# Optimization experiments

Measured on AMD Instinct MI355X. Metric: run time of the kernel, lower is better.

The kernel has to match this reference:

```python
import jax, jax.numpy as jnp
import numpy as np

B, N, DIM, H, HD, MLP = 32, 257, 1024, 16, 64, 4096
SCALE = HD ** -0.5


def _ln(x, w, b, eps=1e-5):
    m = x.mean(-1, keepdims=True)
    v = ((x - m) ** 2).mean(-1, keepdims=True)
    return (x - m) * jax.lax.rsqrt(v + eps) * w + b


def _quick_gelu(x):
    return x * jax.nn.sigmoid(1.702 * x)


def setup_inputs() -> dict:
    key = jax.random.key(0)
    ks = jax.random.split(key, 8)
    p = lambda k, s: jax.random.normal(k, s, jnp.float32) * 0.02
    return {
        'hidden_states': jax.random.normal(ks[0], (B, N, DIM), jnp.float32),
        'ln1_w': jnp.ones((DIM,), jnp.float32), 'ln1_b': jnp.zeros((DIM,), jnp.float32),
        'Wq': p(ks[1], (DIM, DIM)), 'bq': jnp.zeros((DIM,), jnp.float32),
        'Wk': p(ks[2], (DIM, DIM)), 'bk': jnp.zeros((DIM,), jnp.float32),
        'Wv': p(ks[3], (DIM, DIM)), 'bv': jnp.zeros((DIM,), jnp.float32),
        'Wo': p(ks[4], (DIM, DIM)), 'bo': jnp.zeros((DIM,), jnp.float32),
        'ln2_w': jnp.ones((DIM,), jnp.float32), 'ln2_b': jnp.zeros((DIM,), jnp.float32),
        'fc1_w': p(ks[5], (MLP, DIM)), 'fc1_b': jnp.zeros((MLP,), jnp.float32),
        'fc2_w': p(ks[6], (DIM, MLP)), 'fc2_b': jnp.zeros((DIM,), jnp.float32),
    }


def reference(hidden_states, ln1_w, ln1_b, Wq, bq, Wk, bk, Wv, bv, Wo, bo,
              ln2_w, ln2_b, fc1_w, fc1_b, fc2_w, fc2_b):
    x = _ln(hidden_states, ln1_w, ln1_b)            # [B,N,DIM]
    def heads(y):                                    # [B,N,DIM] -> [B,H,N,HD]
        return y.reshape(B, N, H, HD).transpose(0, 2, 1, 3)
    q = heads((x @ Wq.T + bq) * SCALE)
    k = heads(x @ Wk.T + bk)
    v = heads(x @ Wv.T + bv)
    attn_weights = jax.nn.softmax(jnp.einsum('bhnd,bhmd->bhnm', q, k), axis=-1)  # [B,H,N,N]
    ctx = jnp.einsum('bhnm,bhmd->bhnd', attn_weights, v)
    pre_proj = ctx.transpose(0, 2, 1, 3).reshape(B, N, DIM)
    attn_output = pre_proj @ Wo.T + bo
    h = hidden_states + attn_output
    residual = h
    h = _ln(h, ln2_w, ln2_b)
    h = _quick_gelu(h @ fc1_w.T + fc1_b) @ fc2_w.T + fc2_b
    hidden_out = residual + h
    # reuse_start='before_mlp': returns (pre_proj, cache_states=None, hidden, attn_weights, qkvs=None, reuse_map=None)
    return pre_proj, hidden_out, attn_weights
```

## Files before the change

kernel.cpp:

```cpp
#include <hip/hip_runtime.h>

typedef unsigned short u16;
typedef __bf16 bf16x8 __attribute__((ext_vector_type(8)));
typedef float f32x4 __attribute__((ext_vector_type(4)));
typedef unsigned short u16x8 __attribute__((ext_vector_type(8)));
typedef unsigned short u16x4 __attribute__((ext_vector_type(4)));

#define NBATCH 32
#define NTOK   257
#define DMODEL 1024
#define NHEAD  16
#define HDIM   64
#define DMLP   4096
#define MTOK   (NBATCH*NTOK)
#define MPAD   8320

__device__ __forceinline__ u16 f2bf(float f){
    unsigned int u = __float_as_uint(f);
    u = u + 0x7fffu + ((u >> 16) & 1u);
    return (u16)(u >> 16);
}

__device__ __forceinline__ f32x4 mfma16(bf16x8 a, bf16x8 b, f32x4 c){
    return __builtin_amdgcn_mfma_f32_16x16x32_bf16(a, b, c, 0, 0, 0);
}

__device__ __forceinline__ void gload16(const void* g, void* l){
    __builtin_amdgcn_global_load_lds(
        (const __attribute__((address_space(1))) unsigned int*)g,
        (__attribute__((address_space(3))) unsigned int*)l, 16, 0, 0);
}

__device__ __forceinline__ float waveSum64(float v){
    #pragma unroll
    for (int d = 1; d < 64; d <<= 1) v += __shfl_xor(v, d);
    return v;
}

__device__ __forceinline__ void xcd_swz(int &bx, int &by){
    int gx = gridDim.x;
    int nwg = gx * gridDim.y;
    int bid = blockIdx.y * gx + blockIdx.x;
    int wg = (bid & 7) * (nwg >> 3) + (bid >> 3);
    bx = wg % gx; by = wg / gx;
}

__global__ __launch_bounds__(256) void cvt_all(
        const float* __restrict__ wq, const float* __restrict__ wk,
        const float* __restrict__ wv, const float* __restrict__ wo,
        const float* __restrict__ f1, const float* __restrict__ f2,
        u16* __restrict__ dst){
    int b = blockIdx.x;
    const float* s; int rb; float sc = 1.0f;
    if (b < 1024)      { s = wq; rb = 0;    sc = 0.125f; }
    else if (b < 2048) { s = wk; rb = 1024; }
    else if (b < 3072) { s = wv; rb = 2048; }
    else if (b < 4096) { s = wo; rb = 3072; }
    else if (b < 8192) { s = f1; rb = 4096; }
    else               { s = f2; rb = 8192; }
    size_t li = ((size_t)(b - rb)*256 + threadIdx.x)*4;
    float4 v = *(const float4*)(s + li);
    u16x4 o = { f2bf(v.x*sc), f2bf(v.y*sc), f2bf(v.z*sc), f2bf(v.w*sc) };
    *(u16x4*)(dst + (size_t)b*1024 + threadIdx.x*4) = o;
}

__global__ __launch_bounds__(256) void build_bqkv(
        const float* __restrict__ bq, const float* __restrict__ bk,
        const float* __restrict__ bv, float* __restrict__ o){
    int i = blockIdx.x*256 + threadIdx.x;
    float v = (i < 1024) ? bq[i]*0.125f : ((i < 2048) ? bk[i-1024] : bv[i-2048]);
    o[i] = v;
}

__global__ __launch_bounds__(256) void ln_kernel(const float* __restrict__ x,
                                                 const float* __restrict__ w,
                                                 const float* __restrict__ b,
                                                 u16* __restrict__ y){
    int row = blockIdx.x, tid = threadIdx.x;
    float4 v = ((const float4*)(x + (size_t)row*DMODEL))[tid];
    float s = v.x + v.y + v.z + v.w;
    s = waveSum64(s);
    __shared__ float red[8];
    int wv = tid >> 6;
    if ((tid & 63) == 0) red[wv] = s;
    __syncthreads();
    float mean = (red[0]+red[1]+red[2]+red[3]) * (1.0f/1024.0f);
    float dx = v.x-mean, dy = v.y-mean, dz = v.z-mean, dw = v.w-mean;
    float s2 = dx*dx + dy*dy + dz*dz + dw*dw;
    s2 = waveSum64(s2);
    if ((tid & 63) == 0) red[4+wv] = s2;
    __syncthreads();
    float var = (red[4]+red[5]+red[6]+red[7]) * (1.0f/1024.0f);
    float rs = rsqrtf(var + 1e-5f);
    float4 wl = ((const float4*)w)[tid];
    float4 bl = ((const float4*)b)[tid];
    u16x4 o = { f2bf(dx*rs*wl.x + bl.x), f2bf(dy*rs*wl.y + bl.y),
                f2bf(dz*rs*wl.z + bl.z), f2bf(dw*rs*wl.w + bl.w) };
    ((u16x4*)(y + (size_t)row*DMODEL))[tid] = o;
}

template<int EPI>
__global__ __launch_bounds__(256) void gemm_bt(
        const u16* __restrict__ A, const u16* __restrict__ Wt,
        const float* __restrict__ bias, u16* __restrict__ outb,
        int K, int Nn, int Mvalid){
    __shared__ __align__(16) u16 As[128*64];
    __shared__ __align__(16) u16 Bs[128*64];
    int tid = threadIdx.x, lane = tid & 63, w = tid >> 6;
    int wr = w >> 1, wc = w & 1;
    int bx, by; xcd_swz(bx, by);
    int m0 = by*128, n0 = bx*128;
    int lrow = lane & 15, lk = lane >> 4;
    const f32x4 fz = {0.f,0.f,0.f,0.f};
    f32x4 acc[4][4];
    #pragma unroll
    for (int i = 0; i < 4; i++)
        #pragma unroll
        for (int j = 0; j < 4; j++) acc[i][j] = fz;

    const size_t Ks = (size_t)K;
    int so = w*1024 + lane*16;
    for (int kt = 0; kt < K; kt += 64){
        #pragma unroll
        for (int i = 0; i < 4; i++){
            int o = i*4096 + so;
            int row = o >> 7;
            int gsl = ((o >> 4) & 7) ^ (row & 7);
            gload16(A  + (size_t)(m0+row)*Ks + kt + gsl*8, &As[i*2048 + w*512]);
            gload16(Wt + (size_t)(n0+row)*Ks + kt + gsl*8, &Bs[i*2048 + w*512]);
        }
        __syncthreads();
        #pragma unroll
        for (int kk = 0; kk < 2; kk++){
            bf16x8 af[4], bfr[4];
            #pragma unroll
            for (int mi = 0; mi < 4; mi++){
                int row = wr*64 + mi*16 + lrow;
                int sl = (kk*4 + lk) ^ (row & 7);
                af[mi] = *(const bf16x8*)&As[row*64 + sl*8];
            }
            #pragma unroll
            for (int ni = 0; ni < 4; ni++){
                int row = wc*64 + ni*16 + lrow;
                int sl = (kk*4 + lk) ^ (row & 7);
                bfr[ni] = *(const bf16x8*)&Bs[row*64 + sl*8];
            }
            #pragma unroll
            for (int mi = 0; mi < 4; mi++)
                #pragma unroll
                for (int ni = 0; ni < 4; ni++)
                    acc[mi][ni] = mfma16(af[mi], bfr[ni], acc[mi][ni]);
        }
        __syncthreads();
    }
    #pragma unroll
    for (int mi = 0; mi < 4; mi++){
        #pragma unroll
        for (int ni = 0; ni < 4; ni++){
            int col = n0 + wc*64 + ni*16 + lrow;
            float bi = bias[col];
            #pragma unroll
            for (int r = 0; r < 4; r++){
                int row = m0 + wr*64 + mi*16 + lk*4 + r;
                if (row < Mvalid){
                    float v = acc[mi][ni][r] + bi;
                    size_t idx = (size_t)row*Nn + col;
                    if (EPI == 0){
                        outb[idx] = f2bf(v);
                    } else {
                        float g = v / (1.f + __expf(-1.702f*v));
                        outb[idx] = f2bf(g);
                    }
                }
            }
        }
    }
}

__global__ __launch_bounds__(256) void gemm_n64(
        const u16* __restrict__ A, const u16* __restrict__ Wt,
        const float* __restrict__ bias, const float* __restrict__ addsrc,
        float* __restrict__ outf,
        int K, int Nn, int Mvalid){
    __shared__ __align__(16) u16 As[128*64];
    __shared__ __align__(16) u16 Bs[64*64];
    int tid = threadIdx.x, lane = tid & 63, w = tid >> 6;
    int wr = w >> 1, wc = w & 1;
    int bx, by; xcd_swz(bx, by);
    int m0 = by*128, n0 = bx*64;
    int lrow = lane & 15, lk = lane >> 4;
    const f32x4 fz = {0.f,0.f,0.f,0.f};
    f32x4 acc[4][2];
    #pragma unroll
    for (int i = 0; i < 4; i++){ acc[i][0] = fz; acc[i][1] = fz; }

    const size_t Ks = (size_t)K;
    int so = w*1024 + lane*16;
    for (int kt = 0; kt < K; kt += 64){
        #pragma unroll
        for (int i = 0; i < 4; i++){
            int o = i*4096 + so;
            int row = o >> 7;
            int gsl = ((o >> 4) & 7) ^ (row & 7);
            gload16(A + (size_t)(m0+row)*Ks + kt + gsl*8, &As[i*2048 + w*512]);
        }
        #pragma unroll
        for (int i = 0; i < 2; i++){
            int o = i*4096 + so;
            int row = o >> 7;
            int gsl = ((o >> 4) & 7) ^ (row & 7);
            gload16(Wt + (size_t)(n0+row)*Ks + kt + gsl*8, &Bs[i*2048 + w*512]);
        }
        __syncthreads();
        #pragma unroll
        for (int kk = 0; kk < 2; kk++){
            bf16x8 af[4], bfr[2];
            #pragma unroll
            for (int mi = 0; mi < 4; mi++){
                int row = wr*64 + mi*16 + lrow;
                int sl = (kk*4 + lk) ^ (row & 7);
                af[mi] = *(const bf16x8*)&As[row*64 + sl*8];
            }
            #pragma unroll
            for (int ni = 0; ni < 2; ni++){
                int row = wc*32 + ni*16 + lrow;
                int sl = (kk*4 + lk) ^ (row & 7);
                bfr[ni] = *(const bf16x8*)&Bs[row*64 + sl*8];
            }
            #pragma unroll
            for (int mi = 0; mi < 4; mi++)
                #pragma unroll
                for (int ni = 0; ni < 2; ni++)
                    acc[mi][ni] = mfma16(af[mi], bfr[ni], acc[mi][ni]);
        }
        __syncthreads();
    }
    #pragma unroll
    for (int mi = 0; mi < 4; mi++){
        #pragma unroll
        for (int ni = 0; ni < 2; ni++){
            int col = n0 + wc*32 + ni*16 + lrow;
            float bi = bias[col];
            #pragma unroll
            for (int r = 0; r < 4; r++){
                int row = m0 + wr*64 + mi*16 + lk*4 + r;
                if (row < Mvalid){
                    float v = acc[mi][ni][r] + bi;
                    size_t idx = (size_t)row*Nn + col;
                    outf[idx] = addsrc[idx] + v;
                }
            }
        }
    }
}

__global__ __launch_bounds__(256) void attn_kernel(
        const u16* __restrict__ qkv, float* __restrict__ preproj,
        u16* __restrict__ ctxb, float* __restrict__ attnw){
    __shared__ __align__(16) u16 Klds[272*64];
    __shared__ __align__(16) u16 Vt[64*296];
    __shared__ __align__(16) u16 Plds[9*64*32];
    int tid = threadIdx.x, lane = tid & 63, w = tid >> 6;
    int bh = blockIdx.x, bq = bh >> 4, hh = bh & 15;
    int q0 = blockIdx.y*64;
    int lrow = lane & 15, lk = lane >> 4;

    size_t base3 = ((size_t)bq*NTOK)*3072 + hh*HDIM;
    for (int c = tid; c < 2176; c += 256){
        int row = c >> 3, slot = c & 7;
        u16x8 kv = {0,0,0,0,0,0,0,0}, vv = {0,0,0,0,0,0,0,0};
        if (row < NTOK){
            kv = *(const u16x8*)(qkv + base3 + 1024 + (size_t)row*3072 + slot*8);
            vv = *(const u16x8*)(qkv + base3 + 2048 + (size_t)row*3072 + slot*8);
        }
        *(u16x8*)&Klds[row*64 + (slot ^ (row & 7))*8] = kv;
        #pragma unroll
        for (int j = 0; j < 8; j++) Vt[(slot*8 + j)*296 + row] = vv[j];
    }
    for (int i = tid; i < 1024; i += 256) ((unsigned int*)Plds)[8*1024 + i] = 0u;
    for (int i = tid; i < 1536; i += 256){
        int d = i/24, c2 = 272 + (i - d*24);
        Vt[d*296 + c2] = 0;
    }
    int tok = bq*NTOK + q0 + w*16 + lrow;
    const u16* qp = qkv + (size_t)tok*3072 + hh*HDIM;
    bf16x8 qf0 = *(const bf16x8*)(qp + lk*8);
    bf16x8 qf1 = *(const bf16x8*)(qp + 32 + lk*8);
    __syncthreads();

    f32x4 S[17];
    #pragma unroll
    for (int j = 0; j < 17; j++){
        int kcol = j*16 + lrow;
        f32x4 a = {0.f,0.f,0.f,0.f};
        bf16x8 b0 = *(const bf16x8*)&Klds[kcol*64 + ((0 + lk) ^ (kcol & 7))*8];
        a = mfma16(qf0, b0, a);
        bf16x8 b1 = *(const bf16x8*)&Klds[kcol*64 + ((4 + lk) ^ (kcol & 7))*8];
        S[j] = mfma16(qf1, b1, a);
    }
    #pragma unroll
    for (int r = 0; r < 4; r++){
        float mx = -1e30f;
        #pragma unroll
        for (int j = 0; j < 17; j++){
            bool valid = (j < 16) || (lrow == 0);
            mx = fmaxf(mx, valid ? S[j][r] : -1e30f);
        }
        #pragma unroll
        for (int d = 1; d < 16; d <<= 1) mx = fmaxf(mx, __shfl_xor(mx, d));
        float sum = 0.f;
        #pragma unroll
        for (int j = 0; j < 17; j++){
            bool valid = (j < 16) || (lrow == 0);
            float p = valid ? __expf(S[j][r] - mx) : 0.f;
            S[j][r] = p; sum += p;
        }
        #pragma unroll
        for (int d = 1; d < 16; d <<= 1) sum += __shfl_xor(sum, d);
        float inv = 1.f / sum;
        #pragma unroll
        for (int j = 0; j < 17; j++) S[j][r] *= inv;
    }
    #pragma unroll
    for (int r = 0; r < 4; r++){
        int rw = lk*4 + r;
        int qrow = q0 + w*16 + rw;
        bool rowok = qrow < NTOK;
        size_t obase = ((size_t)bh*NTOK + qrow)*NTOK;
        int prow = w*16 + rw;
        #pragma unroll
        for (int j = 0; j < 17; j++){
            int col = j*16 + lrow;
            float p = S[j][r];
            if (rowok && col < NTOK) attnw[obase + col] = p;
            int kstep = col >> 5, koff = col & 31;
            int slot = (koff >> 3) ^ (prow & 3);
            Plds[kstep*2048 + prow*32 + slot*8 + (koff & 7)] = f2bf(p);
        }
    }
    __syncthreads();

    f32x4 C4[4];
    #pragma unroll
    for (int n = 0; n < 4; n++) C4[n] = (f32x4){0.f,0.f,0.f,0.f};
    #pragma unroll
    for (int ks = 0; ks < 9; ks++){
        int prow = w*16 + lrow;
        int slotp = lk ^ (prow & 3);
        bf16x8 pf = *(const bf16x8*)&Plds[ks*2048 + prow*32 + slotp*8];
        #pragma unroll
        for (int n = 0; n < 4; n++){
            int d = n*16 + lrow;
            bf16x8 vf = *(const bf16x8*)&Vt[d*296 + ks*32 + lk*8];
            C4[n] = mfma16(pf, vf, C4[n]);
        }
    }
    #pragma unroll
    for (int n = 0; n < 4; n++){
        #pragma unroll
        for (int r = 0; r < 4; r++){
            int qrow = q0 + w*16 + lk*4 + r;
            if (qrow < NTOK){
                int tok2 = bq*NTOK + qrow;
                int d = hh*HDIM + n*16 + lrow;
                float v = C4[n][r];
                preproj[(size_t)tok2*DMODEL + d] = v;
                ctxb[(size_t)tok2*DMODEL + d] = f2bf(v);
            }
        }
    }
}

extern "C" void kernel_launch(void* const* d_in, const int* in_sizes, int n_in,
                              void* d_out, int out_size, void* d_ws, size_t ws_size,
                              hipStream_t stream){
    const float* hidden = (const float*)d_in[0];
    const float* ln1w = (const float*)d_in[1];
    const float* ln1b = (const float*)d_in[2];
    const float* Wq   = (const float*)d_in[3];
    const float* bq   = (const float*)d_in[4];
    const float* Wk   = (const float*)d_in[5];
    const float* bk   = (const float*)d_in[6];
    const float* Wv   = (const float*)d_in[7];
    const float* bv   = (const float*)d_in[8];
    const float* Wo   = (const float*)d_in[9];
    const float* bo   = (const float*)d_in[10];
    const float* ln2w = (const float*)d_in[11];
    const float* ln2b = (const float*)d_in[12];
    const float* fc1w = (const float*)d_in[13];
    const float* fc1b = (const float*)d_in[14];
    const float* fc2w = (const float*)d_in[15];
    const float* fc2b = (const float*)d_in[16];

    float* out0 = (float*)d_out;
    float* out1 = out0 + (size_t)MTOK*DMODEL;
    float* out2 = out1 + (size_t)MTOK*DMODEL;

    char* ws = (char*)d_ws;
    u16* qkvb = (u16*)ws;
    u16* fc1o = (u16*)ws;
    size_t off = (size_t)MPAD*DMLP*2;
    u16* xln  = (u16*)(ws + off);
    u16* ctxb = xln;
    off += (size_t)MPAD*DMODEL*2;
    u16* wbase = (u16*)(ws + off);
    u16* wqkv = wbase;
    u16* wob  = wbase + 3*1048576;
    u16* wf1  = wbase + 4*1048576;
    u16* wf2  = wbase + 8*1048576;
    off += (size_t)12*1048576*2;
    float* bqkv = (float*)(ws + off);

    cvt_all<<<12288, 256, 0, stream>>>(Wq, Wk, Wv, Wo, fc1w, fc2w, wbase);
    build_bqkv<<<12, 256, 0, stream>>>(bq, bk, bv, bqkv);

    ln_kernel<<<MTOK, 256, 0, stream>>>(hidden, ln1w, ln1b, xln);

    gemm_bt<0><<<dim3(24,65), 256, 0, stream>>>(xln, wqkv, bqkv, qkvb, 1024, 3072, MTOK);

    attn_kernel<<<dim3(512,5), 256, 0, stream>>>(qkvb, out0, ctxb, out2);

    gemm_n64<<<dim3(16,65), 256, 0, stream>>>(ctxb, wob, bo, hidden, out1, 1024, 1024, MTOK);

    ln_kernel<<<MTOK, 256, 0, stream>>>(out1, ln2w, ln2b, xln);

    gemm_bt<2><<<dim3(32,65), 256, 0, stream>>>(xln, wf1, fc1b, fc1o, 1024, 4096, MTOK);

    gemm_n64<<<dim3(16,65), 256, 0, stream>>>(fc1o, wf2, fc2b, out1, out1, 4096, 1024, MTOK);
}
```

Measured before the change: 498.0 us.

## Alias K and P LDS buffers, swizzle V transpose and P layout, add setprio

```diff
diff --git a/kernel.cpp b/kernel.cpp
--- a/kernel.cpp
+++ b/kernel.cpp
@@ -257,9 +257,10 @@
 __global__ __launch_bounds__(256) void attn_kernel(
         const u16* __restrict__ qkv, float* __restrict__ preproj,
         u16* __restrict__ ctxb, float* __restrict__ attnw){
-    __shared__ __align__(16) u16 Klds[272*64];
-    __shared__ __align__(16) u16 Vt[64*296];
-    __shared__ __align__(16) u16 Plds[9*64*32];
+    __shared__ __align__(16) u16 shm[18432 + 64*296];
+    u16* Klds = shm;
+    u16* Plds = shm;
+    u16* Vt   = shm + 18432;
     int tid = threadIdx.x, lane = tid & 63, w = tid >> 6;
     int bh = blockIdx.x, bq = bh >> 4, hh = bh & 15;
     int q0 = blockIdx.y*64;
@@ -274,10 +275,10 @@
             vv = *(const u16x8*)(qkv + base3 + 2048 + (size_t)row*3072 + slot*8);
         }
         *(u16x8*)&Klds[row*64 + (slot ^ (row & 7))*8] = kv;
-        #pragma unroll
-        for (int j = 0; j < 8; j++) Vt[(slot*8 + j)*296 + row] = vv[j];
-    }
-    for (int i = tid; i < 1024; i += 256) ((unsigned int*)Plds)[8*1024 + i] = 0u;
+        int vr = (row < 256) ? (row ^ (slot << 3)) : row;
+        #pragma unroll
+        for (int j = 0; j < 8; j++) Vt[(slot*8 + j)*296 + vr] = vv[j];
+    }
     for (int i = tid; i < 1536; i += 256){
         int d = i/24, c2 = 272 + (i - d*24);
         Vt[d*296 + c2] = 0;
@@ -289,6 +290,7 @@
     __syncthreads();
 
     f32x4 S[17];
+    __builtin_amdgcn_s_setprio(1);
     #pragma unroll
     for (int j = 0; j < 17; j++){
         int kcol = j*16 + lrow;
@@ -298,6 +300,7 @@
         bf16x8 b1 = *(const bf16x8*)&Klds[kcol*64 + ((4 + lk) ^ (kcol & 7))*8];
         S[j] = mfma16(qf1, b1, a);
     }
+    __builtin_amdgcn_s_setprio(0);
     #pragma unroll
     for (int r = 0; r < 4; r++){
         float mx = -1e30f;
@@ -320,6 +323,14 @@
         float inv = 1.f / sum;
         #pragma unroll
         for (int j = 0; j < 17; j++) S[j][r] *= inv;
+    }
+    __syncthreads();
+
+    for (int idx = tid; idx < 1024; idx += 256){
+        int prow = idx >> 4, kk = idx & 15;
+        int koff = 16 + kk;
+        int slot = ((koff >> 3) ^ (prow >> 2)) & 3;
+        Plds[8*2048 + prow*32 + slot*8 + (koff & 7)] = 0;
     }
     #pragma unroll
     for (int r = 0; r < 4; r++){
@@ -334,7 +345,7 @@
             float p = S[j][r];
             if (rowok && col < NTOK) attnw[obase + col] = p;
             int kstep = col >> 5, koff = col & 31;
-            int slot = (koff >> 3) ^ (prow & 3);
+            int slot = ((koff >> 3) ^ (prow >> 2)) & 3;
             Plds[kstep*2048 + prow*32 + slot*8 + (koff & 7)] = f2bf(p);
         }
     }
@@ -343,18 +354,23 @@
     f32x4 C4[4];
     #pragma unroll
     for (int n = 0; n < 4; n++) C4[n] = (f32x4){0.f,0.f,0.f,0.f};
+    __builtin_amdgcn_s_setprio(1);
     #pragma unroll
     for (int ks = 0; ks < 9; ks++){
         int prow = w*16 + lrow;
-        int slotp = lk ^ (prow & 3);
+        int slotp = (lk ^ (lrow >> 2)) & 3;
         bf16x8 pf = *(const bf16x8*)&Plds[ks*2048 + prow*32 + slotp*8];
         #pragma unroll
         for (int n = 0; n < 4; n++){
             int d = n*16 + lrow;
-            bf16x8 vf = *(const bf16x8*)&Vt[d*296 + ks*32 + lk*8];
+            int xv = (d >> 3) & 7;
+            int kbase = ks*32 + lk*8;
+            int kl = (ks < 8) ? (kbase ^ (xv << 3)) : kbase;
+            bf16x8 vf = *(const bf16x8*)&Vt[d*296 + kl];
             C4[n] = mfma16(pf, vf, C4[n]);
         }
     }
+    __builtin_amdgcn_s_setprio(0);
     #pragma unroll
     for (int n = 0; n < 4; n++){
         #pragma unroll
```

Result: faster. 470.2 us (-5.6%).
